# Optimization experiments

Measured on AMD Instinct MI355X. Metric: run time of the kernel, lower is better.

Reference implementation:

```python
import jax, jax.numpy as jnp
import numpy as np

B, K, D = 2048, 100000, 50  # batch, memory-bank size (num users), USER_VEC_DIM

def setup_inputs() -> dict:
    key = jax.random.key(0)
    k1, k2 = jax.random.split(key)
    x = jax.random.normal(k1, (B, D), dtype=jnp.float32)   # batch of user vectors
    M = jax.random.normal(k2, (K, D), dtype=jnp.float32)   # user_memory_vec bank
    return {"x": x, "M": M}

def reference(x, M):
    # Batched form of the per-item Python loop in call():
    #   mu = M @ u ; gamma = softmax(mu, axis=0) ; u_ = sum_k gamma_k * M[k]
    scores = jnp.einsum('bd,kd->bk', x, M)           # [B, K]
    attn = jax.nn.softmax(scores, axis=-1)           # softmax over memory slots
    u_ = jnp.einsum('bk,kd->bd', attn, M)            # attention readout [B, D]
    return jnp.concatenate([x, u_], axis=-1)         # [B, 2D]
```

## Files before the change

### kernel.cpp

```cpp
#include <hip/hip_runtime.h>
#include <hip/hip_bf16.h>
#include <math.h>

#define B_SZ 2048
#define K_SZ 100000
#define D_SZ 50
#define BT   64
#define CK   64
#define STR  72
#define MTS  78
#define SHIFT 30.0f
#define LOG2E 1.4426950408889634f
#define SHIFT_L2 43.280851226668905f
#define PSTRIDE 52
#define NCH   1563
#define IMG_CH 9216
#define IMG_BYTES ((size_t)NCH * IMG_CH * 2)
#define NSEG  18
#define PART_BYTES ((size_t)B_SZ * PSTRIDE * sizeof(float))

typedef short short8 __attribute__((ext_vector_type(8)));
typedef short short4v __attribute__((ext_vector_type(4)));
typedef float f32x4 __attribute__((ext_vector_type(4)));

__device__ __forceinline__ unsigned short bf16_rne(float f) {
    union { float f; unsigned int u; } v; v.f = f;
    unsigned int r = (v.u + 0x7fffu + ((v.u >> 16) & 1u)) >> 16;
    return (unsigned short)r;
}
__device__ __forceinline__ float bf16_to_f(unsigned short h) {
    union { unsigned int u; float f; } v; v.u = ((unsigned int)h) << 16;
    return v.f;
}

__device__ __forceinline__ void load_lds16(const void* g, void* l) {
    __builtin_amdgcn_global_load_lds(
        (const __attribute__((address_space(1))) unsigned int*)g,
        (__attribute__((address_space(3))) unsigned int*)l, 16, 0, 0);
}

__global__ __launch_bounds__(256)
void precompute_m(const float* __restrict__ M, unsigned short* __restrict__ img) {
    __shared__ __align__(16) unsigned short Mt[64 * MTS];
    const int t = threadIdx.x;
    const int c0 = blockIdx.x;
    const int k0 = c0 * 64;
    for (int i = t; i < (64 * MTS) / 2; i += 256) ((unsigned int*)Mt)[i] = 0;
    __syncthreads();
    unsigned int* gh = (unsigned int*)(img + (size_t)c0 * IMG_CH);
    for (int i = t; i < 64 * 36; i += 256) {
        int r = i / 36, cd = i - r * 36, c = cd * 2;
        int kg = k0 + r;
        unsigned int val = 0;
        if (kg < K_SZ && c < D_SZ) {
            float2 v = *(const float2*)&M[(size_t)kg * D_SZ + c];
            val = ((unsigned int)bf16_rne(v.y) << 16) | bf16_rne(v.x);
            Mt[c * MTS + r]       = (unsigned short)(val & 0xffffu);
            Mt[(c + 1) * MTS + r] = (unsigned short)(val >> 16);
        }
        gh[i] = val;
    }
    __syncthreads();
    unsigned int* gt = (unsigned int*)(img + (size_t)c0 * IMG_CH + 64 * STR);
    for (int i = t; i < 64 * 36; i += 256) {
        int r = i / 36, c = i - r * 36;
        gt[i] = *(const unsigned int*)&Mt[r * MTS + c * 2];
    }
}

__global__ __launch_bounds__(512, 4)
void attend_fast(const float* __restrict__ x, const unsigned short* __restrict__ img,
                 float* __restrict__ part, int slice) {
    __shared__ __align__(16) unsigned short lds[4 * IMG_CH];
    __shared__ float lsc[4][64];

    const int t = threadIdx.x;
    const int w = t >> 6, lane = t & 63;
    const int quad = lane >> 4, lq = lane & 15;

    const int bid = blockIdx.x;
    const int rr = bid >> 3;
    const int split = (rr >> 5) * 8 + (bid & 7);
    const int xtile = rr & 31;
    const int b0 = xtile * BT;
    const int kbeg = split * slice;
    const int kend = min(kbeg + slice, K_SZ);

    const int nt0 = (w & 1) * 2;
    const int mblk = w >> 1;

    short8 xh[2][2], xl[2][2];
    for (int j = 0; j < 2; ++j) {
        int row = b0 + (nt0 + j) * 16 + lq;
        const float* xr = x + (size_t)row * D_SZ;
        for (int ki = 0; ki < 2; ++ki) {
            int d0 = ki * 32 + quad * 8;
            float v[8];
#pragma unroll
            for (int e = 0; e < 8; ++e) v[e] = 0.f;
            if (d0 + 8 <= D_SZ) {
#pragma unroll
                for (int e = 0; e < 4; ++e) {
                    float2 f2 = *(const float2*)&xr[d0 + 2 * e];
                    v[2 * e] = f2.x; v[2 * e + 1] = f2.y;
                }
            } else if (d0 < D_SZ) {
                float2 f2 = *(const float2*)&xr[d0];
                v[0] = f2.x; v[1] = f2.y;
            }
            short8 sh, sl;
#pragma unroll
            for (int e = 0; e < 8; ++e) {
                unsigned short h = bf16_rne(v[e]);
                sh[e] = (short)h;
                sl[e] = (short)bf16_rne(v[e] - bf16_to_f(h));
            }
            xh[j][ki] = sh; xl[j][ki] = sl;
        }
    }

    f32x4 Uacc[2][4] = {};
    float lac[2] = {0.f, 0.f};

    const int ci0 = kbeg >> 6;
    const int nch = (kend - kbeg + CK - 1) / CK;
    const int r0 = bid % nch;

    {
        const unsigned short* g = img + (size_t)(ci0 + r0) * IMG_CH;
        for (int seg = w; seg < NSEG; seg += 8)
            load_lds16((const unsigned int*)(g + seg * 512) + lane * 4, lds + seg * 512);
        if (nch > 1) {
            int c1 = r0 + 1; if (c1 >= nch) c1 -= nch;
            const unsigned short* g1 = img + (size_t)(ci0 + c1) * IMG_CH;
            for (int seg = w; seg < NSEG; seg += 8)
                load_lds16((const unsigned int*)(g1 + seg * 512) + lane * 4,
                           lds + IMG_CH + seg * 512);
        }
    }

    const int aoff0 = (mblk * 16 + lq) * STR + quad * 8;
    const int boffb = mblk * 16 + quad * 4;

    for (int n = 0; n < nch; n += 2) {
        __builtin_amdgcn_s_waitcnt(0);
        __syncthreads();
#pragma unroll
        for (int f = 2; f <= 3; ++f) {
            int nn = n + f;
            if (nn < nch) {
                int cc = r0 + nn; if (cc >= nch) cc -= nch;
                const unsigned short* g = img + (size_t)(ci0 + cc) * IMG_CH;
                unsigned short* dst = lds + (size_t)(nn & 3) * IMG_CH;
                for (int seg = w; seg < NSEG; seg += 8)
                    load_lds16((const unsigned int*)(g + seg * 512) + lane * 4,
                               dst + seg * 512);
            }
        }

        const int hasB = (n + 1 < nch);
        const unsigned short* MhiA = lds + (size_t)(n & 3) * IMG_CH;
        const unsigned short* MtA  = MhiA + 64 * STR;
        const unsigned short* MhiB = lds + (size_t)((n + 1) & 3) * IMG_CH;
        const unsigned short* MtB  = MhiB + 64 * STR;

        unsigned int paA[2][2];
        {
            f32x4 S[2] = {};
#pragma unroll
            for (int ki = 0; ki < 2; ++ki) {
                short8 ah = *(const short8*)&MhiA[aoff0 + ki * 32];
#pragma unroll
                for (int j = 0; j < 2; ++j) {
                    S[j] = __builtin_amdgcn_mfma_f32_16x16x32_bf16(ah, xh[j][ki], S[j], 0, 0, 0);
                    S[j] = __builtin_amdgcn_mfma_f32_16x16x32_bf16(ah, xl[j][ki], S[j], 0, 0, 0);
                }
            }
#pragma unroll
            for (int j = 0; j < 2; ++j) {
                float p0 = __builtin_amdgcn_exp2f(fmaf(S[j][0], LOG2E, -SHIFT_L2));
                float p1 = __builtin_amdgcn_exp2f(fmaf(S[j][1], LOG2E, -SHIFT_L2));
                float p2 = __builtin_amdgcn_exp2f(fmaf(S[j][2], LOG2E, -SHIFT_L2));
                float p3 = __builtin_amdgcn_exp2f(fmaf(S[j][3], LOG2E, -SHIFT_L2));
                lac[j] += (p0 + p1) + (p2 + p3);
                __hip_bfloat162 q01 = __float22bfloat162_rn(make_float2(p0, p1));
                __hip_bfloat162 q23 = __float22bfloat162_rn(make_float2(p2, p3));
                __builtin_memcpy(&paA[j][0], &q01, 4);
                __builtin_memcpy(&paA[j][1], &q23, 4);
            }
        }

        unsigned int paB[2][2] = {{0u, 0u}, {0u, 0u}};
        if (hasB) {
            f32x4 S[2] = {};
#pragma unroll
            for (int ki = 0; ki < 2; ++ki) {
                short8 ah = *(const short8*)&MhiB[aoff0 + ki * 32];
#pragma unroll
                for (int j = 0; j < 2; ++j) {
                    S[j] = __builtin_amdgcn_mfma_f32_16x16x32_bf16(ah, xh[j][ki], S[j], 0, 0, 0);
                    S[j] = __builtin_amdgcn_mfma_f32_16x16x32_bf16(ah, xl[j][ki], S[j], 0, 0, 0);
                }
            }
#pragma unroll
            for (int j = 0; j < 2; ++j) {
                float p0 = __builtin_amdgcn_exp2f(fmaf(S[j][0], LOG2E, -SHIFT_L2));
                float p1 = __builtin_amdgcn_exp2f(fmaf(S[j][1], LOG2E, -SHIFT_L2));
                float p2 = __builtin_amdgcn_exp2f(fmaf(S[j][2], LOG2E, -SHIFT_L2));
                float p3 = __builtin_amdgcn_exp2f(fmaf(S[j][3], LOG2E, -SHIFT_L2));
                lac[j] += (p0 + p1) + (p2 + p3);
                __hip_bfloat162 q01 = __float22bfloat162_rn(make_float2(p0, p1));
                __hip_bfloat162 q23 = __float22bfloat162_rn(make_float2(p2, p3));
                __builtin_memcpy(&paB[j][0], &q01, 4);
                __builtin_memcpy(&paB[j][1], &q23, 4);
            }
        }

#pragma unroll
        for (int dt = 0; dt < 4; ++dt) {
            int boff = (dt * 16 + lq) * STR + boffb;
            union { short8 s8; unsigned int u[4]; } bm;
            bm.u[0] = *(const unsigned int*)&MtA[boff];
            bm.u[1] = *(const unsigned int*)&MtA[boff + 2];
            bm.u[2] = *(const unsigned int*)&MtB[boff];
            bm.u[3] = *(const unsigned int*)&MtB[boff + 2];
#pragma unroll
            for (int j = 0; j < 2; ++j) {
                union { short8 s8; unsigned int u[4]; } pa;
                pa.u[0] = paA[j][0]; pa.u[1] = paA[j][1];
                pa.u[2] = paB[j][0]; pa.u[3] = paB[j][1];
                Uacc[j][dt] = __builtin_amdgcn_mfma_f32_16x16x32_bf16(pa.s8, bm.s8, Uacc[j][dt], 0, 0, 0);
            }
        }
    }

    for (int j = 0; j < 2; ++j) {
        float v = lac[j];
        v += __shfl_xor(v, 16);
        v += __shfl_xor(v, 32);
        if (quad == 0) lsc[mblk][(nt0 + j) * 16 + lq] = v;
    }

    float* Ured = (float*)lds;
#pragma unroll
    for (int rnd = 0; rnd < 4; ++rnd) {
        __syncthreads();
        if (mblk == rnd) {
#pragma unroll
            for (int j = 0; j < 2; ++j)
#pragma unroll
                for (int dt = 0; dt < 4; ++dt)
#pragma unroll
                    for (int r4 = 0; r4 < 4; ++r4) {
                        int row = (nt0 + j) * 16 + quad * 4 + r4;
                        int col = dt * 16 + lq;
                        if (rnd == 0) Ured[row * 66 + col] = Uacc[j][dt][r4];
                        else          Ured[row * 66 + col] += Uacc[j][dt][r4];
                    }
        }
    }
    __syncthreads();

    float* pp = part + (size_t)b0 * PSTRIDE;
    for (int i = t; i < BT * D_SZ; i += 512) {
        int row = i / D_SZ, d = i - row * D_SZ;
        atomicAdd(&pp[(size_t)row * PSTRIDE + d], Ured[row * 66 + d]);
    }
    if (t < BT) {
        float Ls = lsc[0][t] + lsc[1][t] + lsc[2][t] + lsc[3][t];
        atomicAdd(&pp[(size_t)t * PSTRIDE + D_SZ], Ls);
    }
}

__global__ __launch_bounds__(512, 4)
void attend_partial_v2(const float* __restrict__ x, const float* __restrict__ M,
                       float* __restrict__ part, int slice) {
    __shared__ __align__(16) unsigned short lds[4 * 64 * STR];
    __shared__ float lsc[4][64];
    unsigned short* bufA  = lds;
    unsigned short* bufB  = lds + 64 * STR;
    unsigned short* Mc_hi = lds + 2 * 64 * STR;
    unsigned short* Mc_lo = lds + 3 * 64 * STR;

    const int t = threadIdx.x;
    const int w = t >> 6, lane = t & 63;
    const int quad = lane >> 4, lq = lane & 15;
    const int b0 = blockIdx.x * 64;
    const int split = blockIdx.y;
    const int kbeg = split * slice;
    const int kend = min(kbeg + slice, K_SZ);

    for (int i = t; i < 4 * 64 * STR; i += 512) lds[i] = 0;
    __syncthreads();
    for (int i = t; i < 64 * 25; i += 512) {
        int r = i / 25, cp = i - r * 25, c = cp * 2;
        float2 v = *(const float2*)&x[(size_t)(b0 + r) * D_SZ + c];
        unsigned short h0 = bf16_rne(v.x), h1 = bf16_rne(v.y);
        unsigned short l0 = bf16_rne(v.x - bf16_to_f(h0));
        unsigned short l1 = bf16_rne(v.y - bf16_to_f(h1));
        *(unsigned int*)&bufA[r * STR + c] = ((unsigned int)h1 << 16) | h0;
        *(unsigned int*)&bufB[r * STR + c] = ((unsigned int)l1 << 16) | l0;
    }
    __syncthreads();

    const int nt0 = (w & 1) * 2;
    const int mblk = w >> 1;
    short8 xh[2][2], xl[2][2];
    for (int j = 0; j < 2; ++j)
        for (int ki = 0; ki < 2; ++ki) {
            int off = ((nt0 + j) * 16 + lq) * STR + ki * 32 + quad * 8;
            xh[j][ki] = *(const short8*)&bufA[off];
            xl[j][ki] = *(const short8*)&bufB[off];
        }

    f32x4 Uacc[2] = {};
    float lac[2] = {0.f, 0.f};

    for (int k0 = kbeg; k0 < kend; k0 += CK) {
        __syncthreads();
        for (int i = t; i < 64 * 25; i += 512) {
            int r = i / 25, cp = i - r * 25, c = cp * 2;
            int kg = k0 + r;
            float2 v = make_float2(0.f, 0.f);
            if (kg < kend) v = *(const float2*)&M[(size_t)kg * D_SZ + c];
            unsigned short h0 = bf16_rne(v.x), h1 = bf16_rne(v.y);
            unsigned short l0 = bf16_rne(v.x - bf16_to_f(h0));
            unsigned short l1 = bf16_rne(v.y - bf16_to_f(h1));
            *(unsigned int*)&Mc_hi[r * STR + c] = ((unsigned int)h1 << 16) | h0;
            *(unsigned int*)&Mc_lo[r * STR + c] = ((unsigned int)l1 << 16) | l0;
            bufB[c * STR + r] = h0;
            bufB[(c + 1) * STR + r] = h1;
        }
        __syncthreads();

        f32x4 S[2] = {};
        for (int ki = 0; ki < 2; ++ki) {
            int aoff = (mblk * 16 + lq) * STR + ki * 32 + quad * 8;
            short8 ah = *(const short8*)&Mc_hi[aoff];
            short8 al = *(const short8*)&Mc_lo[aoff];
            for (int j = 0; j < 2; ++j) {
                S[j] = __builtin_amdgcn_mfma_f32_16x16x32_bf16(ah, xh[j][ki], S[j], 0, 0, 0);
                S[j] = __builtin_amdgcn_mfma_f32_16x16x32_bf16(ah, xl[j][ki], S[j], 0, 0, 0);
                S[j] = __builtin_amdgcn_mfma_f32_16x16x32_bf16(al, xh[j][ki], S[j], 0, 0, 0);
            }
        }
        for (int j = 0; j < 2; ++j) {
            unsigned short pb4[4];
#pragma unroll
            for (int r4 = 0; r4 < 4; ++r4) {
                float p = __expf(S[j][r4] - SHIFT);
                lac[j] += p;
                pb4[r4] = bf16_rne(p);
            }
            int b = (nt0 + j) * 16 + lq;
            int n0 = mblk * 16 + quad * 4;
            *(unsigned int*)&bufA[b * STR + n0]     = ((unsigned int)pb4[1] << 16) | pb4[0];
            *(unsigned int*)&bufA[b * STR + n0 + 2] = ((unsigned int)pb4[3] << 16) | pb4[2];
        }
        __syncthreads();
        for (int ki = 0; ki < 2; ++ki) {
            int poff = (mblk * 16 + lq) * STR + ki * 32 + quad * 8;
            short8 ap = *(const short8*)&bufA[poff];
            for (int j = 0; j < 2; ++j) {
                int doff = ((nt0 + j) * 16 + lq) * STR + ki * 32 + quad * 8;
                short8 bm = *(const short8*)&bufB[doff];
                Uacc[j] = __builtin_amdgcn_mfma_f32_16x16x32_bf16(ap, bm, Uacc[j], 0, 0, 0);
            }
        }
    }

    for (int j = 0; j < 2; ++j) {
        float v = lac[j];
        v += __shfl_xor(v, 16);
        v += __shfl_xor(v, 32);
        if (quad == 0) lsc[mblk][(nt0 + j) * 16 + lq] = v;
    }
    __syncthreads();
    float* pp = part + ((size_t)split * B_SZ + b0) * PSTRIDE;
    for (int j = 0; j < 2; ++j) {
        int d = (nt0 + j) * 16 + lq;
        if (d < D_SZ) {
#pragma unroll
            for (int r4 = 0; r4 < 4; ++r4) {
                int b = mblk * 16 + quad * 4 + r4;
                pp[(size_t)b * PSTRIDE + d] = Uacc[j][r4];
            }
        }
    }
    if (t < 64) {
        float Ls = lsc[0][t] + lsc[1][t] + lsc[2][t] + lsc[3][t];
        pp[(size_t)t * PSTRIDE + D_SZ] = Ls;
    }
}

__global__ __launch_bounds__(256)
void combine_norm(const float* __restrict__ x, const float* __restrict__ part,
                  float* __restrict__ out) {
    const int b = blockIdx.x * 4 + (threadIdx.x >> 6);
    const int t = threadIdx.x & 63;
    if (t < D_SZ) {
        float L = part[(size_t)b * PSTRIDE + D_SZ];
        float acc = part[(size_t)b * PSTRIDE + t];
        out[(size_t)b * (2 * D_SZ) + t] = x[(size_t)b * D_SZ + t];
        out[(size_t)b * (2 * D_SZ) + D_SZ + t] = acc / L;
    }
}

__global__ __launch_bounds__(256)
void combine(const float* __restrict__ x, const float* __restrict__ part,
             float* __restrict__ out, int nsplit) {
    const int b = blockIdx.x * 4 + (threadIdx.x >> 6);
    const int t = threadIdx.x & 63;
    float L = 0.f;
    for (int s = 0; s < nsplit; ++s)
        L += part[((size_t)s * B_SZ + b) * PSTRIDE + D_SZ];
    if (t < D_SZ) {
        float acc = 0.f;
        for (int s = 0; s < nsplit; ++s)
            acc += part[((size_t)s * B_SZ + b) * PSTRIDE + t];
        out[(size_t)b * (2 * D_SZ) + t] = x[(size_t)b * D_SZ + t];
        out[(size_t)b * (2 * D_SZ) + D_SZ + t] = acc / L;
    }
}

extern "C" void kernel_launch(void* const* d_in, const int* in_sizes, int n_in,
                              void* d_out, int out_size, void* d_ws, size_t ws_size,
                              hipStream_t stream) {
    const float* x = (const float*)d_in[0];
    const float* M = (const float*)d_in[1];
    float* out = (float*)d_out;
    const size_t per_split = (size_t)B_SZ * PSTRIDE * sizeof(float);

    if (ws_size >= IMG_BYTES + PART_BYTES) {
        unsigned short* img = (unsigned short*)d_ws;
        float* part = (float*)((char*)d_ws + IMG_BYTES);
        const int ns = 32;
        int slice = (((K_SZ + ns - 1) / ns) + 127) & ~127;
        precompute_m<<<NCH, 256, 0, stream>>>(M, img);
        hipMemsetAsync(part, 0, PART_BYTES, stream);
        attend_fast<<<32 * ns, 512, 0, stream>>>(x, img, part, slice);
        combine_norm<<<B_SZ / 4, 256, 0, stream>>>(x, part, out);
    } else {
        float* part = (float*)d_ws;
        int ns = (int)(ws_size / per_split);
        if (ns > 32) ns = 32;
        if (ns < 1) ns = 1;
        int slice = (K_SZ + ns - 1) / ns;
        dim3 gridA(B_SZ / 64, ns);
        attend_partial_v2<<<gridA, 512, 0, stream>>>(x, M, part, slice);
        combine<<<B_SZ / 4, 256, 0, stream>>>(x, part, out, ns);
    }
}
```

Baseline: 176.5 us.

## Load M chunks directly into registers instead of LDS staging; fold memset into precompute

Drops the 4-deep LDS ring buffer filled by global_load_lds, so each wave now reads its A and B fragments of the M image straight from global memory into registers, prefetching the next two chunks while MFMAs run. Block-wide barriers in the main loop go away and LDS use shrinks to the reduction buffer, which may allow more resident blocks. The partial-sum zeroing moves into the precompute kernel, removing a separate memset launch. The cost is redundant global/L2 traffic (each wave re-reads data that was previously shared through LDS) and a staggered start offset (r0) that is no longer used. The odd-chunk tail also now reuses stale B fragments multiplied by zero probabilities.

```diff
diff --git a/kernel.cpp b/kernel.cpp
--- a/kernel.cpp
+++ b/kernel.cpp
@@ -16,7 +16,6 @@
 #define NCH   1563
 #define IMG_CH 9216
 #define IMG_BYTES ((size_t)NCH * IMG_CH * 2)
-#define NSEG  18
 #define PART_BYTES ((size_t)B_SZ * PSTRIDE * sizeof(float))
 
 typedef short short8 __attribute__((ext_vector_type(8)));
@@ -33,18 +32,14 @@
     return v.f;
 }
 
-__device__ __forceinline__ void load_lds16(const void* g, void* l) {
-    __builtin_amdgcn_global_load_lds(
-        (const __attribute__((address_space(1))) unsigned int*)g,
-        (__attribute__((address_space(3))) unsigned int*)l, 16, 0, 0);
-}
-
 __global__ __launch_bounds__(256)
-void precompute_m(const float* __restrict__ M, unsigned short* __restrict__ img) {
+void precompute_m(const float* __restrict__ M, unsigned short* __restrict__ img,
+                  float* __restrict__ part) {
     __shared__ __align__(16) unsigned short Mt[64 * MTS];
     const int t = threadIdx.x;
     const int c0 = blockIdx.x;
     const int k0 = c0 * 64;
+    for (int i = c0 * 256 + t; i < B_SZ * PSTRIDE; i += NCH * 256) part[i] = 0.f;
     for (int i = t; i < (64 * MTS) / 2; i += 256) ((unsigned int*)Mt)[i] = 0;
     __syncthreads();
     unsigned int* gh = (unsigned int*)(img + (size_t)c0 * IMG_CH);
@@ -68,10 +63,36 @@
     }
 }
 
+__device__ __forceinline__ void ph1exp(const short8 (&ah)[2],
+                                       const short8 (&xh)[2][2], const short8 (&xl)[2][2],
+                                       float (&lac)[2], unsigned int (&pa)[2][2]) {
+    f32x4 S[2] = {};
+#pragma unroll
+    for (int ki = 0; ki < 2; ++ki) {
+#pragma unroll
+        for (int j = 0; j < 2; ++j) {
+            S[j] = __builtin_amdgcn_mfma_f32_16x16x32_bf16(ah[ki], xh[j][ki], S[j], 0, 0, 0);
+            S[j] = __builtin_amdgcn_mfma_f32_16x16x32_bf16(ah[ki], xl[j][ki], S[j], 0, 0, 0);
+        }
+    }
+#pragma unroll
+    for (int j = 0; j < 2; ++j) {
+        float p0 = __builtin_amdgcn_exp2f(fmaf(S[j][0], LOG2E, -SHIFT_L2));
+        float p1 = __builtin_amdgcn_exp2f(fmaf(S[j][1], LOG2E, -SHIFT_L2));
+        float p2 = __builtin_amdgcn_exp2f(fmaf(S[j][2], LOG2E, -SHIFT_L2));
+        float p3 = __builtin_amdgcn_exp2f(fmaf(S[j][3], LOG2E, -SHIFT_L2));
+        lac[j] += (p0 + p1) + (p2 + p3);
+        __hip_bfloat162 q01 = __float22bfloat162_rn(make_float2(p0, p1));
+        __hip_bfloat162 q23 = __float22bfloat162_rn(make_float2(p2, p3));
+        __builtin_memcpy(&pa[j][0], &q01, 4);
+        __builtin_memcpy(&pa[j][1], &q23, 4);
+    }
+}
+
 __global__ __launch_bounds__(512, 4)
 void attend_fast(const float* __restrict__ x, const unsigned short* __restrict__ img,
                  float* __restrict__ part, int slice) {
-    __shared__ __align__(16) unsigned short lds[4 * IMG_CH];
+    __shared__ float Ured[64 * 66];
     __shared__ float lsc[4][64];
 
     const int t = threadIdx.x;
@@ -124,106 +145,49 @@
 
     const int ci0 = kbeg >> 6;
     const int nch = (kend - kbeg + CK - 1) / CK;
-    const int r0 = bid % nch;
+    const unsigned short* g0 = img + (size_t)ci0 * IMG_CH;
+
+    const int aoff0 = (mblk * 16 + lq) * STR + quad * 8;
+    const int boff0 = 64 * STR + lq * STR + mblk * 16 + quad * 4;
+
+    short8 ahA[2], ahB[2];
+    short4v bmA[4], bmB[4];
 
     {
-        const unsigned short* g = img + (size_t)(ci0 + r0) * IMG_CH;
-        for (int seg = w; seg < NSEG; seg += 8)
-            load_lds16((const unsigned int*)(g + seg * 512) + lane * 4, lds + seg * 512);
-        if (nch > 1) {
-            int c1 = r0 + 1; if (c1 >= nch) c1 -= nch;
-            const unsigned short* g1 = img + (size_t)(ci0 + c1) * IMG_CH;
-            for (int seg = w; seg < NSEG; seg += 8)
-                load_lds16((const unsigned int*)(g1 + seg * 512) + lane * 4,
-                           lds + IMG_CH + seg * 512);
-        }
-    }
-
-    const int aoff0 = (mblk * 16 + lq) * STR + quad * 8;
-    const int boffb = mblk * 16 + quad * 4;
-
-    for (int n = 0; n < nch; n += 2) {
-        __builtin_amdgcn_s_waitcnt(0);
-        __syncthreads();
-#pragma unroll
-        for (int f = 2; f <= 3; ++f) {
-            int nn = n + f;
-            if (nn < nch) {
-                int cc = r0 + nn; if (cc >= nch) cc -= nch;
-                const unsigned short* g = img + (size_t)(ci0 + cc) * IMG_CH;
-                unsigned short* dst = lds + (size_t)(nn & 3) * IMG_CH;
-                for (int seg = w; seg < NSEG; seg += 8)
-                    load_lds16((const unsigned int*)(g + seg * 512) + lane * 4,
-                               dst + seg * 512);
-            }
-        }
-
-        const int hasB = (n + 1 < nch);
-        const unsigned short* MhiA = lds + (size_t)(n & 3) * IMG_CH;
-        const unsigned short* MtA  = MhiA + 64 * STR;
-        const unsigned short* MhiB = lds + (size_t)((n + 1) & 3) * IMG_CH;
-        const unsigned short* MtB  = MhiB + 64 * STR;
-
-        unsigned int paA[2][2];
+        const unsigned short* gA = g0;
+        const unsigned short* gB = g0 + (size_t)(nch > 1 ? 1 : 0) * IMG_CH;
+        ahA[0] = *(const short8*)&gA[aoff0];
+        ahA[1] = *(const short8*)&gA[aoff0 + 32];
+        ahB[0] = *(const short8*)&gB[aoff0];
+        ahB[1] = *(const short8*)&gB[aoff0 + 32];
+#pragma unroll
+        for (int dt = 0; dt < 4; ++dt) {
+            bmA[dt] = *(const short4v*)&gA[boff0 + dt * 16 * STR];
+            bmB[dt] = *(const short4v*)&gB[boff0 + dt * 16 * STR];
+        }
+    }
+
+    int n = 0;
+    for (; n + 2 <= nch; n += 2) {
+        unsigned int paA[2][2], paB[2][2];
+        ph1exp(ahA, xh, xl, lac, paA);
+        ph1exp(ahB, xh, xl, lac, paB);
+
         {
-            f32x4 S[2] = {};
-#pragma unroll
-            for (int ki = 0; ki < 2; ++ki) {
-                short8 ah = *(const short8*)&MhiA[aoff0 + ki * 32];
-#pragma unroll
-                for (int j = 0; j < 2; ++j) {
-                    S[j] = __builtin_amdgcn_mfma_f32_16x16x32_bf16(ah, xh[j][ki], S[j], 0, 0, 0);
-                    S[j] = __builtin_amdgcn_mfma_f32_16x16x32_bf16(ah, xl[j][ki], S[j], 0, 0, 0);
-                }
-            }
-#pragma unroll
-            for (int j = 0; j < 2; ++j) {
-                float p0 = __builtin_amdgcn_exp2f(fmaf(S[j][0], LOG2E, -SHIFT_L2));
-                float p1 = __builtin_amdgcn_exp2f(fmaf(S[j][1], LOG2E, -SHIFT_L2));
-                float p2 = __builtin_amdgcn_exp2f(fmaf(S[j][2], LOG2E, -SHIFT_L2));
-                float p3 = __builtin_amdgcn_exp2f(fmaf(S[j][3], LOG2E, -SHIFT_L2));
-                lac[j] += (p0 + p1) + (p2 + p3);
-                __hip_bfloat162 q01 = __float22bfloat162_rn(make_float2(p0, p1));
-                __hip_bfloat162 q23 = __float22bfloat162_rn(make_float2(p2, p3));
-                __builtin_memcpy(&paA[j][0], &q01, 4);
-                __builtin_memcpy(&paA[j][1], &q23, 4);
-            }
-        }
-
-        unsigned int paB[2][2] = {{0u, 0u}, {0u, 0u}};
-        if (hasB) {
-            f32x4 S[2] = {};
-#pragma unroll
-            for (int ki = 0; ki < 2; ++ki) {
-                short8 ah = *(const short8*)&MhiB[aoff0 + ki * 32];
-#pragma unroll
-                for (int j = 0; j < 2; ++j) {
-                    S[j] = __builtin_amdgcn_mfma_f32_16x16x32_bf16(ah, xh[j][ki], S[j], 0, 0, 0);
-                    S[j] = __builtin_amdgcn_mfma_f32_16x16x32_bf16(ah, xl[j][ki], S[j], 0, 0, 0);
-                }
-            }
-#pragma unroll
-            for (int j = 0; j < 2; ++j) {
-                float p0 = __builtin_amdgcn_exp2f(fmaf(S[j][0], LOG2E, -SHIFT_L2));
-                float p1 = __builtin_amdgcn_exp2f(fmaf(S[j][1], LOG2E, -SHIFT_L2));
-                float p2 = __builtin_amdgcn_exp2f(fmaf(S[j][2], LOG2E, -SHIFT_L2));
-                float p3 = __builtin_amdgcn_exp2f(fmaf(S[j][3], LOG2E, -SHIFT_L2));
-                lac[j] += (p0 + p1) + (p2 + p3);
-                __hip_bfloat162 q01 = __float22bfloat162_rn(make_float2(p0, p1));
-                __hip_bfloat162 q23 = __float22bfloat162_rn(make_float2(p2, p3));
-                __builtin_memcpy(&paB[j][0], &q01, 4);
-                __builtin_memcpy(&paB[j][1], &q23, 4);
-            }
+            int n2 = (n + 2 < nch) ? n + 2 : nch - 1;
+            int n3 = (n + 3 < nch) ? n + 3 : nch - 1;
+            const unsigned short* gA2 = g0 + (size_t)n2 * IMG_CH;
+            const unsigned short* gB2 = g0 + (size_t)n3 * IMG_CH;
+            ahA[0] = *(const short8*)&gA2[aoff0];
+            ahA[1] = *(const short8*)&gA2[aoff0 + 32];
+            ahB[0] = *(const short8*)&gB2[aoff0];
+            ahB[1] = *(const short8*)&gB2[aoff0 + 32];
         }
 
 #pragma unroll
         for (int dt = 0; dt < 4; ++dt) {
-            int boff = (dt * 16 + lq) * STR + boffb;
-            union { short8 s8; unsigned int u[4]; } bm;
-            bm.u[0] = *(const unsigned int*)&MtA[boff];
-            bm.u[1] = *(const unsigned int*)&MtA[boff + 2];
-            bm.u[2] = *(const unsigned int*)&MtB[boff];
-            bm.u[3] = *(const unsigned int*)&MtB[boff + 2];
+            union { short8 s8; short4v h[2]; } bm;
+            bm.h[0] = bmA[dt]; bm.h[1] = bmB[dt];
 #pragma unroll
             for (int j = 0; j < 2; ++j) {
                 union { short8 s8; unsigned int u[4]; } pa;
@@ -232,6 +196,35 @@
                 Uacc[j][dt] = __builtin_amdgcn_mfma_f32_16x16x32_bf16(pa.s8, bm.s8, Uacc[j][dt], 0, 0, 0);
             }
         }
+
+        {
+            int n2 = (n + 2 < nch) ? n + 2 : nch - 1;
+            int n3 = (n + 3 < nch) ? n + 3 : nch - 1;
+            const unsigned short* gA2 = g0 + (size_t)n2 * IMG_CH;
+            const unsigned short* gB2 = g0 + (size_t)n3 * IMG_CH;
+#pragma unroll
+            for (int dt = 0; dt < 4; ++dt) {
+                bmA[dt] = *(const short4v*)&gA2[boff0 + dt * 16 * STR];
+                bmB[dt] = *(const short4v*)&gB2[boff0 + dt * 16 * STR];
+            }
+        }
+    }
+
+    if (n < nch) {
+        unsigned int paA[2][2];
+        ph1exp(ahA, xh, xl, lac, paA);
+#pragma unroll
+        for (int dt = 0; dt < 4; ++dt) {
+            union { short8 s8; short4v h[2]; } bm;
+            bm.h[0] = bmA[dt]; bm.h[1] = bmB[dt];
+#pragma unroll
+            for (int j = 0; j < 2; ++j) {
+                union { short8 s8; unsigned int u[4]; } pa;
+                pa.u[0] = paA[j][0]; pa.u[1] = paA[j][1];
+                pa.u[2] = 0u; pa.u[3] = 0u;
+                Uacc[j][dt] = __builtin_amdgcn_mfma_f32_16x16x32_bf16(pa.s8, bm.s8, Uacc[j][dt], 0, 0, 0);
+            }
+        }
     }
 
     for (int j = 0; j < 2; ++j) {
@@ -241,7 +234,6 @@
         if (quad == 0) lsc[mblk][(nt0 + j) * 16 + lq] = v;
     }
 
-    float* Ured = (float*)lds;
 #pragma unroll
     for (int rnd = 0; rnd < 4; ++rnd) {
         __syncthreads();
@@ -436,8 +428,7 @@
         float* part = (float*)((char*)d_ws + IMG_BYTES);
         const int ns = 32;
         int slice = (((K_SZ + ns - 1) / ns) + 127) & ~127;
-        precompute_m<<<NCH, 256, 0, stream>>>(M, img);
-        hipMemsetAsync(part, 0, PART_BYTES, stream);
+        precompute_m<<<NCH, 256, 0, stream>>>(M, img, part);
         attend_fast<<<32 * ns, 512, 0, stream>>>(x, img, part, slice);
         combine_norm<<<B_SZ / 4, 256, 0, stream>>>(x, part, out);
     } else {
```

Result: slower. 222.7 us (+26.2%).

## Fold partial-buffer zeroing into precompute and fuse final normalization via last-block counter

Applied to the files above, without the earlier changes.

The separate memset of the partial buffer is moved into the precompute kernel, and the combine_norm kernel is removed. Instead, each attention block bumps a per-tile atomic counter after its atomic accumulation, and the last block for a tile reads back the sums and writes the normalized output plus the copied x. This cuts two launches from the pipeline, at the cost of extra fences and serialized tail work in the last block per tile.

```diff
diff --git a/kernel.cpp b/kernel.cpp
--- a/kernel.cpp
+++ b/kernel.cpp
@@ -40,11 +40,14 @@
 }
 
 __global__ __launch_bounds__(256)
-void precompute_m(const float* __restrict__ M, unsigned short* __restrict__ img) {
+void precompute_m(const float* __restrict__ M, unsigned short* __restrict__ img,
+                  float* __restrict__ part, unsigned int* __restrict__ cnt) {
     __shared__ __align__(16) unsigned short Mt[64 * MTS];
     const int t = threadIdx.x;
     const int c0 = blockIdx.x;
     const int k0 = c0 * 64;
+    for (int i = c0 * 256 + t; i < B_SZ * PSTRIDE; i += NCH * 256) part[i] = 0.f;
+    if (c0 == 0 && t < 32) cnt[t] = 0u;
     for (int i = t; i < (64 * MTS) / 2; i += 256) ((unsigned int*)Mt)[i] = 0;
     __syncthreads();
     unsigned int* gh = (unsigned int*)(img + (size_t)c0 * IMG_CH);
@@ -70,9 +73,12 @@
 
 __global__ __launch_bounds__(512, 4)
 void attend_fast(const float* __restrict__ x, const unsigned short* __restrict__ img,
-                 float* __restrict__ part, int slice) {
+                 float* __restrict__ part, unsigned int* __restrict__ cnt,
+                 float* __restrict__ out, int slice, int nsplit) {
     __shared__ __align__(16) unsigned short lds[4 * IMG_CH];
     __shared__ float lsc[4][64];
+    __shared__ float Lrow[64];
+    __shared__ int lastFlag;
 
     const int t = threadIdx.x;
     const int w = t >> 6, lane = t & 63;
@@ -269,6 +275,26 @@
     if (t < BT) {
         float Ls = lsc[0][t] + lsc[1][t] + lsc[2][t] + lsc[3][t];
         atomicAdd(&pp[(size_t)t * PSTRIDE + D_SZ], Ls);
+    }
+
+    __threadfence();
+    __syncthreads();
+    if (t == 0) {
+        unsigned int old = atomicAdd(&cnt[xtile], 1u);
+        lastFlag = (old == (unsigned int)(nsplit - 1));
+    }
+    __syncthreads();
+    if (lastFlag) {
+        __threadfence();
+        if (t < BT) Lrow[t] = atomicAdd(&pp[(size_t)t * PSTRIDE + D_SZ], 0.f);
+        __syncthreads();
+        for (int i = t; i < BT * D_SZ; i += 512) {
+            int row = i / D_SZ, d = i - row * D_SZ;
+            int gb = b0 + row;
+            float acc = atomicAdd(&pp[(size_t)row * PSTRIDE + d], 0.f);
+            out[(size_t)gb * (2 * D_SZ) + d] = x[(size_t)gb * D_SZ + d];
+            out[(size_t)gb * (2 * D_SZ) + D_SZ + d] = acc / Lrow[row];
+        }
     }
 }
 
@@ -390,19 +416,6 @@
     if (t < 64) {
         float Ls = lsc[0][t] + lsc[1][t] + lsc[2][t] + lsc[3][t];
         pp[(size_t)t * PSTRIDE + D_SZ] = Ls;
-    }
-}
-
-__global__ __launch_bounds__(256)
-void combine_norm(const float* __restrict__ x, const float* __restrict__ part,
-                  float* __restrict__ out) {
-    const int b = blockIdx.x * 4 + (threadIdx.x >> 6);
-    const int t = threadIdx.x & 63;
-    if (t < D_SZ) {
-        float L = part[(size_t)b * PSTRIDE + D_SZ];
-        float acc = part[(size_t)b * PSTRIDE + t];
-        out[(size_t)b * (2 * D_SZ) + t] = x[(size_t)b * D_SZ + t];
-        out[(size_t)b * (2 * D_SZ) + D_SZ + t] = acc / L;
     }
 }
 
@@ -431,15 +444,14 @@
     float* out = (float*)d_out;
     const size_t per_split = (size_t)B_SZ * PSTRIDE * sizeof(float);
 
-    if (ws_size >= IMG_BYTES + PART_BYTES) {
+    if (ws_size >= IMG_BYTES + PART_BYTES + 128) {
         unsigned short* img = (unsigned short*)d_ws;
         float* part = (float*)((char*)d_ws + IMG_BYTES);
+        unsigned int* cnt = (unsigned int*)((char*)d_ws + IMG_BYTES + PART_BYTES);
         const int ns = 32;
         int slice = (((K_SZ + ns - 1) / ns) + 127) & ~127;
-        precompute_m<<<NCH, 256, 0, stream>>>(M, img);
-        hipMemsetAsync(part, 0, PART_BYTES, stream);
-        attend_fast<<<32 * ns, 512, 0, stream>>>(x, img, part, slice);
-        combine_norm<<<B_SZ / 4, 256, 0, stream>>>(x, part, out);
+        precompute_m<<<NCH, 256, 0, stream>>>(M, img, part, cnt);
+        attend_fast<<<32 * ns, 512, 0, stream>>>(x, img, part, cnt, out, slice, ns);
     } else {
         float* part = (float*)d_ws;
         int ns = (int)(ws_size / per_split);
```

Result: slower. 301.8 us (+71.0%).
